# Optimization experiments

Measured on AMD Instinct MI355X. Metric: run time of the kernel, lower is better.

## Reference

```python
import jax, jax.numpy as jnp
import numpy as np

N_NODES = 100000
N_EDGES = 1600000
D = 128
BN_EPS = 1e-5

def setup_inputs() -> dict:
    key = jax.random.key(0)
    ks = jax.random.split(key, 6)
    h = jax.random.normal(ks[0], (N_NODES, D), dtype=jnp.float32)
    src = jax.random.randint(ks[1], (N_EDGES,), 0, N_NODES, dtype=jnp.int32)
    dst = jax.random.randint(ks[2], (N_EDGES,), 0, N_NODES, dtype=jnp.int32)
    eps = jnp.zeros((1,), dtype=jnp.float32)
    # 2-layer GIN apply_func MLP, scaled for stable activations
    W1 = jax.random.normal(ks[3], (D, D), dtype=jnp.float32) / np.sqrt(D)
    b1 = jnp.zeros((D,), dtype=jnp.float32)
    W2 = jax.random.normal(ks[4], (D, D), dtype=jnp.float32) / np.sqrt(D)
    b2 = jnp.zeros((D,), dtype=jnp.float32)
    gamma = jnp.ones((D,), dtype=jnp.float32)
    beta = jnp.zeros((D,), dtype=jnp.float32)
    return {"h": h, "src": src, "dst": dst, "eps": eps,
            "W1": W1, "b1": b1, "W2": W2, "b2": b2,
            "gamma": gamma, "beta": beta}

def reference(h, src, dst, eps, W1, b1, W2, b2, gamma, beta):
    # --- neighbor sum aggregation: update_all(copy_u('h'), fn.sum) ---
    msgs = h[src]                                   # [E, D] irregular gather
    neigh = jax.ops.segment_sum(msgs, dst, num_segments=N_NODES)  # [N, D]
    # --- eps-scaled self term ---
    x = (1.0 + eps[0]) * h + neigh                  # [N, D]
    # --- apply_func: 2-layer MLP ---
    x = jax.nn.relu(x @ W1 + b1)
    x = x @ W2 + b2
    # --- BatchNorm1d over node dim (training-mode batch stats) ---
    mean = jnp.mean(x, axis=0)
    var = jnp.mean(jnp.square(x - mean), axis=0)
    x = (x - mean) * jax.lax.rsqrt(var + BN_EPS) * gamma + beta
    # --- activation + residual ---
    x = jax.nn.relu(x)
    x = h + x  # residual (in_dim == out_dim)
    return x
```

## Files before the change

kernel.cpp:

```cpp
#include <hip/hip_runtime.h>

#define NN 100000
#define NE 1600000
#define DD 128
#define BN_EPS 1e-5f

#define NWIN 782
#define NWINP 1024
#define EPB 8192
#define NBLK ((NE + EPB - 1) / EPB)
#define CAP 3072
#define PREPBLKS 828
#define GRID_PS (NBLK + PREPBLKS)
#define BN_BLOCKS 1024

typedef __attribute__((ext_vector_type(8))) short short8;
typedef __attribute__((ext_vector_type(4))) float floatx4;

__device__ __forceinline__ unsigned short f2bf(float f) {
    union { float f; unsigned u; } v; v.f = f;
    return (unsigned short)((v.u + 0x7FFFu + ((v.u >> 16) & 1u)) >> 16);
}
__device__ __forceinline__ float bf2f(unsigned short u) {
    union { unsigned u; float f; } v; v.u = ((unsigned)u) << 16;
    return v.f;
}

__global__ __launch_bounds__(256) void prep_scatter_kernel(
    float* __restrict__ stats,
    const float* __restrict__ W1, const float* __restrict__ W2,
    unsigned short* __restrict__ W1t, unsigned short* __restrict__ W2t,
    const float* __restrict__ h, unsigned short* __restrict__ hb, int do_hb,
    const int* __restrict__ src, const int* __restrict__ dst,
    int* __restrict__ wcnt, int* __restrict__ estage)
{
    __shared__ int lofs[NWINP];
    __shared__ int lcur[NWINP];
    __shared__ int gbase[NWINP];
    __shared__ int sorted[EPB];
    __shared__ int stmp[256];
    int t = threadIdx.x;

    if (blockIdx.x < NBLK) {
        int blk = blockIdx.x;
        for (int w = t; w < NWINP; w += 256) lcur[w] = 0;
        __syncthreads();
        int base = blk * EPB;
        int cnt = min(EPB, NE - base);
        for (int i = t; i < cnt; i += 256)
            atomicAdd(&lcur[dst[base + i] >> 7], 1);
        __syncthreads();

        int w0 = t * 4;
        int c0 = lcur[w0], c1 = lcur[w0 + 1], c2 = lcur[w0 + 2], c3 = lcur[w0 + 3];
        int tsum = c0 + c1 + c2 + c3;
        stmp[t] = tsum;
        __syncthreads();
#pragma unroll
        for (int ofs = 1; ofs < 256; ofs <<= 1) {
            int u = (t >= ofs) ? stmp[t - ofs] : 0;
            __syncthreads();
            stmp[t] += u;
            __syncthreads();
        }
        int excl = stmp[t] - tsum;
        lofs[w0]     = excl;
        lofs[w0 + 1] = excl + c0;
        lofs[w0 + 2] = excl + c0 + c1;
        lofs[w0 + 3] = excl + c0 + c1 + c2;
        int gb0 = (w0     < NWIN && c0) ? atomicAdd(&wcnt[w0],     c0) : 0;
        int gb1 = (w0 + 1 < NWIN && c1) ? atomicAdd(&wcnt[w0 + 1], c1) : 0;
        int gb2 = (w0 + 2 < NWIN && c2) ? atomicAdd(&wcnt[w0 + 2], c2) : 0;
        int gb3 = (w0 + 3 < NWIN && c3) ? atomicAdd(&wcnt[w0 + 3], c3) : 0;
        gbase[w0]     = w0 * CAP + gb0;
        gbase[w0 + 1] = (w0 + 1) * CAP + gb1;
        gbase[w0 + 2] = (w0 + 2) * CAP + gb2;
        gbase[w0 + 3] = (w0 + 3) * CAP + gb3;
        lcur[w0] = lofs[w0]; lcur[w0 + 1] = lofs[w0 + 1];
        lcur[w0 + 2] = lofs[w0 + 2]; lcur[w0 + 3] = lofs[w0 + 3];
        __syncthreads();

        for (int i = t; i < cnt; i += 256) {
            int d = dst[base + i];
            int s = src[base + i];
            int p = atomicAdd(&lcur[d >> 7], 1);
            sorted[p] = (s << 7) | (d & 127);
        }
        __syncthreads();

        for (int w = t; w < NWIN; w += 256) {
            int lb = lofs[w], le = lcur[w];
            int g = gbase[w];
            for (int j = lb; j < le; ++j)
                estage[g + (j - lb)] = sorted[j];
        }
    } else {
        int tid0 = (blockIdx.x - NBLK) * 256 + t;
        int stride = PREPBLKS * 256;
        if (tid0 < 2 * DD) stats[tid0] = 0.0f;
        for (int i = tid0; i < DD * DD; i += stride) {
            int n = i >> 7, k = i & 127;
            W1t[i] = f2bf(W1[k * DD + n]);
            W2t[i] = f2bf(W2[k * DD + n]);
        }
        if (do_hb) {
            const float4* h4 = (const float4*)h;
            ushort4* hb4 = (ushort4*)hb;
            for (int i = tid0; i < NN * (DD / 4); i += stride) {
                float4 v = h4[i];
                ushort4 o;
                o.x = f2bf(v.x); o.y = f2bf(v.y); o.z = f2bf(v.z); o.w = f2bf(v.w);
                hb4[i] = o;
            }
        }
    }
}

template <bool HB>
__global__ __launch_bounds__(256) void permgather_kernel(
    const float* __restrict__ h, const unsigned short* __restrict__ hb,
    const float* __restrict__ eps, const int* __restrict__ wcnt,
    const int* __restrict__ estage, unsigned short* __restrict__ xb)
{
    __shared__ int es[CAP];
    __shared__ int cnt[128];
    __shared__ int beg[128];
    __shared__ int cur[128];
    __shared__ int dh[64];
    __shared__ int dcur[64];
    __shared__ unsigned char order[128];

    int b = blockIdx.x, t = threadIdx.x;
    if (t < 128) cnt[t] = 0;
    if (t < 64) dh[t] = 0;
    __syncthreads();

    int n = min(wcnt[b], CAP);
    int wbase = b * CAP;
    for (int i = t; i < n; i += 256)
        atomicAdd(&cnt[estage[wbase + i] & 127], 1);
    __syncthreads();

    if (t < 128) beg[t] = cnt[t];
    __syncthreads();
#pragma unroll
    for (int ofs = 1; ofs < 128; ofs <<= 1) {
        int u = (t < 128 && t >= ofs) ? beg[t - ofs] : 0;
        __syncthreads();
        if (t < 128) beg[t] += u;
        __syncthreads();
    }
    if (t < 128) {
        int ex = beg[t] - cnt[t];
        beg[t] = ex;
        cur[t] = ex;
        atomicAdd(&dh[min(cnt[t], 63)], 1);
    }
    __syncthreads();

    if (t < 64) dcur[t] = dh[t];
    __syncthreads();
#pragma unroll
    for (int ofs = 1; ofs < 64; ofs <<= 1) {
        int u = (t < 64 && t >= ofs) ? dcur[t - ofs] : 0;
        __syncthreads();
        if (t < 64) dcur[t] += u;
        __syncthreads();
    }
    if (t < 64) dcur[t] -= dh[t];
    __syncthreads();
    if (t < 128) {
        int p = atomicAdd(&dcur[min(cnt[t], 63)], 1);
        order[p] = (unsigned char)t;
    }
    __syncthreads();

    for (int i = t; i < n; i += 256) {
        int e = estage[wbase + i];
        int p = atomicAdd(&cur[e & 127], 1);
        es[p] = e >> 7;
    }
    __syncthreads();

    const float sE = 1.0f + eps[0];
    const float4* h4 = (const float4*)h;
    const short8* hb8 = (const short8*)hb;
    int c8 = t & 15;
#pragma unroll
    for (int pass = 0; pass < 8; ++pass) {
        int nl = order[pass * 16 + (t >> 4)];
        int node = (b << 7) + nl;
        if (node >= NN) continue;
        float4 a0 = h4[node * 32 + c8 * 2];
        float4 a1 = h4[node * 32 + c8 * 2 + 1];
        float acc[8] = {sE * a0.x, sE * a0.y, sE * a0.z, sE * a0.w,
                        sE * a1.x, sE * a1.y, sE * a1.z, sE * a1.w};
        int e = beg[nl], eend = beg[nl] + cnt[nl];
        if (HB) {
            for (; e + 3 < eend; e += 4) {
                int s0 = es[e], s1 = es[e + 1], s2 = es[e + 2], s3 = es[e + 3];
                short8 v0 = hb8[s0 * 16 + c8];
                short8 v1 = hb8[s1 * 16 + c8];
                short8 v2 = hb8[s2 * 16 + c8];
                short8 v3 = hb8[s3 * 16 + c8];
#pragma unroll
                for (int j = 0; j < 8; ++j) {
                    float t0 = bf2f((unsigned short)v0[j]) + bf2f((unsigned short)v1[j]);
                    float t1 = bf2f((unsigned short)v2[j]) + bf2f((unsigned short)v3[j]);
                    acc[j] += t0 + t1;
                }
            }
            for (; e < eend; ++e) {
                short8 v0 = hb8[es[e] * 16 + c8];
#pragma unroll
                for (int j = 0; j < 8; ++j) acc[j] += bf2f((unsigned short)v0[j]);
            }
        } else {
            for (; e + 1 < eend; e += 2) {
                int s0 = es[e], s1 = es[e + 1];
                float4 u0 = h4[s0 * 32 + c8 * 2], u1 = h4[s0 * 32 + c8 * 2 + 1];
                float4 w0 = h4[s1 * 32 + c8 * 2], w1 = h4[s1 * 32 + c8 * 2 + 1];
                acc[0] += u0.x + w0.x; acc[1] += u0.y + w0.y;
                acc[2] += u0.z + w0.z; acc[3] += u0.w + w0.w;
                acc[4] += u1.x + w1.x; acc[5] += u1.y + w1.y;
                acc[6] += u1.z + w1.z; acc[7] += u1.w + w1.w;
            }
            if (e < eend) {
                int s0 = es[e];
                float4 u0 = h4[s0 * 32 + c8 * 2], u1 = h4[s0 * 32 + c8 * 2 + 1];
                acc[0] += u0.x; acc[1] += u0.y; acc[2] += u0.z; acc[3] += u0.w;
                acc[4] += u1.x; acc[5] += u1.y; acc[6] += u1.z; acc[7] += u1.w;
            }
        }
        short8 o;
#pragma unroll
        for (int j = 0; j < 8; ++j) o[j] = (short)f2bf(acc[j]);
        ((short8*)xb)[node * 16 + c8] = o;
    }
}

__global__ __launch_bounds__(256) void mlp_fused_kernel(
    const unsigned short* __restrict__ X,
    const unsigned short* __restrict__ W1t, const unsigned short* __restrict__ W2t,
    const float* __restrict__ b1, const float* __restrict__ b2,
    unsigned short* __restrict__ Y, float* __restrict__ stats)
{
    extern __shared__ char smem[];
    unsigned short* wl = (unsigned short*)smem;
    unsigned short* xl = (unsigned short*)(smem + 34816);

    const int tid = threadIdx.x;
    const int r0 = blockIdx.x * 64;
    const int lane = tid & 63;
    const int wv = tid >> 6;
    const int m = lane & 15;
    const int hi = lane >> 4;

    const short8* W18 = (const short8*)W1t;
#pragma unroll
    for (int l = 0; l < 8; ++l) {
        int idx = tid + l * 256;
        int n = idx >> 4, c = idx & 15;
        *(short8*)&wl[n * 136 + c * 8] = W18[idx];
    }
    const short8* X8 = (const short8*)X;
#pragma unroll
    for (int l = 0; l < 4; ++l) {
        int idx = tid + l * 256;
        int row = idx >> 4, c = idx & 15;
        int g = r0 + row;
        short8 v = {0, 0, 0, 0, 0, 0, 0, 0};
        if (g < NN) v = X8[g * 16 + c];
        *(short8*)&xl[row * 136 + c * 8] = v;
    }
    __syncthreads();

    floatx4 acc[8];
#pragma unroll
    for (int i = 0; i < 8; ++i) acc[i] = (floatx4){0.f, 0.f, 0.f, 0.f};
#pragma unroll
    for (int kc = 0; kc < 4; ++kc) {
        short8 a = *(const short8*)&xl[(wv * 16 + m) * 136 + kc * 32 + hi * 8];
#pragma unroll
        for (int nt = 0; nt < 8; ++nt) {
            short8 b = *(const short8*)&wl[(nt * 16 + m) * 136 + kc * 32 + hi * 8];
            acc[nt] = __builtin_amdgcn_mfma_f32_16x16x32_bf16(a, b, acc[nt], 0, 0, 0);
        }
    }
    __syncthreads();

#pragma unroll
    for (int nt = 0; nt < 8; ++nt) {
        float bv = b1[nt * 16 + m];
#pragma unroll
        for (int r = 0; r < 4; ++r) {
            float v = fmaxf(acc[nt][r] + bv, 0.f);
            xl[(wv * 16 + hi * 4 + r) * 136 + nt * 16 + m] = f2bf(v);
        }
    }
    const short8* W28 = (const short8*)W2t;
#pragma unroll
    for (int l = 0; l < 8; ++l) {
        int idx = tid + l * 256;
        int n = idx >> 4, c = idx & 15;
        *(short8*)&wl[n * 136 + c * 8] = W28[idx];
    }
    __syncthreads();

#pragma unroll
    for (int i = 0; i < 8; ++i) acc[i] = (floatx4){0.f, 0.f, 0.f, 0.f};
#pragma unroll
    for (int kc = 0; kc < 4; ++kc) {
        short8 a = *(const short8*)&xl[(wv * 16 + m) * 136 + kc * 32 + hi * 8];
#pragma unroll
        for (int nt = 0; nt < 8; ++nt) {
            short8 b = *(const short8*)&wl[(nt * 16 + m) * 136 + kc * 32 + hi * 8];
            acc[nt] = __builtin_amdgcn_mfma_f32_16x16x32_bf16(a, b, acc[nt], 0, 0, 0);
        }
    }
    __syncthreads();

#pragma unroll
    for (int nt = 0; nt < 8; ++nt) {
        float bv = b2[nt * 16 + m];
#pragma unroll
        for (int r = 0; r < 4; ++r) {
            float v = acc[nt][r] + bv;
            xl[(wv * 16 + hi * 4 + r) * 136 + nt * 16 + m] = f2bf(v);
        }
    }
    __syncthreads();

#pragma unroll
    for (int l = 0; l < 4; ++l) {
        int idx = tid + l * 256;
        int row = idx >> 4, c = idx & 15;
        int g = r0 + row;
        if (g < NN)
            ((short8*)Y)[g * 16 + c] = *(const short8*)&xl[row * 136 + c * 8];
    }

    int col = tid & 127, half = tid >> 7;
    int rlim = min(64, NN - r0);
    int rbeg = half * 32, rend = min(rbeg + 32, rlim);
    float s = 0.f, q = 0.f;
    for (int r = rbeg; r < rend; ++r) {
        float v = bf2f(xl[r * 136 + col]);
        s += v; q += v * v;
    }
    float* red = (float*)wl;
    red[tid] = s;
    red[256 + tid] = q;
    __syncthreads();
    if (half == 0) {
        atomicAdd(&stats[col],      red[col] + red[128 + col]);
        atomicAdd(&stats[DD + col], red[256 + col] + red[256 + 128 + col]);
    }
}

__global__ __launch_bounds__(256) void bn_final_kernel(
    const unsigned short* __restrict__ Y, const float* __restrict__ h,
    const float* __restrict__ gamma, const float* __restrict__ beta,
    const float* __restrict__ stats, float* __restrict__ out)
{
    const float invN = 1.0f / (float)NN;
    int t0 = blockIdx.x * 256 + threadIdx.x;
    int c8 = t0 & 15;
    float sc[8], sh[8];
#pragma unroll
    for (int j = 0; j < 8; ++j) {
        int col = c8 * 8 + j;
        float mu = stats[col] * invN;
        float var = stats[DD + col] * invN - mu * mu;
        float s = rsqrtf(var + BN_EPS) * gamma[col];
        sc[j] = s;
        sh[j] = beta[col] - mu * s;
    }
    const short8* Y8 = (const short8*)Y;
    const float4* H4 = (const float4*)h;
    float4* O4 = (float4*)out;
    const int total = NN * 16;
    const int stride = BN_BLOCKS * 256;
    for (int i = t0; i < total; i += stride) {
        short8 u = Y8[i];
        float4 h0 = H4[2 * i], h1 = H4[2 * i + 1];
        float4 r0, r1;
        r0.x = h0.x + fmaxf(bf2f((unsigned short)u[0]) * sc[0] + sh[0], 0.f);
        r0.y = h0.y + fmaxf(bf2f((unsigned short)u[1]) * sc[1] + sh[1], 0.f);
        r0.z = h0.z + fmaxf(bf2f((unsigned short)u[2]) * sc[2] + sh[2], 0.f);
        r0.w = h0.w + fmaxf(bf2f((unsigned short)u[3]) * sc[3] + sh[3], 0.f);
        r1.x = h1.x + fmaxf(bf2f((unsigned short)u[4]) * sc[4] + sh[4], 0.f);
        r1.y = h1.y + fmaxf(bf2f((unsigned short)u[5]) * sc[5] + sh[5], 0.f);
        r1.z = h1.z + fmaxf(bf2f((unsigned short)u[6]) * sc[6] + sh[6], 0.f);
        r1.w = h1.w + fmaxf(bf2f((unsigned short)u[7]) * sc[7] + sh[7], 0.f);
        O4[2 * i] = r0;
        O4[2 * i + 1] = r1;
    }
}

extern "C" void kernel_launch(void* const* d_in, const int* in_sizes, int n_in,
                              void* d_out, int out_size, void* d_ws, size_t ws_size,
                              hipStream_t stream)
{
    const float* h     = (const float*)d_in[0];
    const int*   src   = (const int*)d_in[1];
    const int*   dst   = (const int*)d_in[2];
    const float* eps   = (const float*)d_in[3];
    const float* W1    = (const float*)d_in[4];
    const float* b1    = (const float*)d_in[5];
    const float* W2    = (const float*)d_in[6];
    const float* b2    = (const float*)d_in[7];
    const float* gamma = (const float*)d_in[8];
    const float* beta  = (const float*)d_in[9];
    float* out = (float*)d_out;

    char* w = (char*)d_ws;
    size_t o = 0;
    float* stats    = (float*)(w + o); o += 256 * 4;
    int* wcnt       = (int*)(w + o); o += 1024 * 4;
    unsigned short* W1t = (unsigned short*)(w + o); o += (size_t)DD * DD * 2;
    unsigned short* W2t = (unsigned short*)(w + o); o += (size_t)DD * DD * 2;
    int* estage     = (int*)(w + o); o += (size_t)NWIN * CAP * 4;
    unsigned short* xb  = (unsigned short*)(w + o); o += (size_t)NN * DD * 2;
    unsigned short* hb  = (unsigned short*)(w + o); o += (size_t)NN * DD * 2;
    const int use_hb = (ws_size >= o) ? 1 : 0;

    hipMemsetAsync(wcnt, 0, 1024 * sizeof(int), stream);

    prep_scatter_kernel<<<GRID_PS, 256, 0, stream>>>(
        stats, W1, W2, W1t, W2t, h, hb, use_hb, src, dst, wcnt, estage);

    if (use_hb)
        permgather_kernel<true><<<NWIN, 256, 0, stream>>>(h, hb, eps, wcnt, estage, xb);
    else
        permgather_kernel<false><<<NWIN, 256, 0, stream>>>(h, hb, eps, wcnt, estage, xb);

    int gemm_blocks = (NN + 63) / 64;
    size_t gemm_lds = 34816 + 17408;
    mlp_fused_kernel<<<gemm_blocks, 256, gemm_lds, stream>>>(xb, W1t, W2t, b1, b2, xb, stats);

    bn_final_kernel<<<BN_BLOCKS, 256, 0, stream>>>(xb, h, gamma, beta, stats, out);
}
```

Measured before the change: 296.6 us.

## Fuse neighbor gather with MLP GEMMs using 64-node windows

Destination windows shrink from 128 to 64 nodes so each gather block's output tile matches the MLP's 64-row tile. The gathered bf16 rows stay in LDS and feed both MFMA GEMMs directly, which removes the intermediate xb write/read round trip and one kernel launch. Weights are staged in two 64-row halves to fit LDS, and BN statistics are now accumulated from fp32 values instead of rounded bf16. The trade-off is twice as many scatter windows with a smaller per-window capacity (1536 edges), so an unusually dense window could overflow, and the gather and GEMM phases now share a single block's resources.

```diff
diff --git a/kernel.cpp b/kernel.cpp
--- a/kernel.cpp
+++ b/kernel.cpp
@@ -5,11 +5,13 @@
 #define DD 128
 #define BN_EPS 1e-5f
 
-#define NWIN 782
-#define NWINP 1024
+#define WSH 6
+#define WSZ 64
+#define NWIN ((NN + WSZ - 1) / WSZ)
+#define NWINP 2048
 #define EPB 8192
 #define NBLK ((NE + EPB - 1) / EPB)
-#define CAP 3072
+#define CAP 1536
 #define PREPBLKS 828
 #define GRID_PS (NBLK + PREPBLKS)
 #define BN_BLOCKS 1024
@@ -48,12 +50,14 @@
         int base = blk * EPB;
         int cnt = min(EPB, NE - base);
         for (int i = t; i < cnt; i += 256)
-            atomicAdd(&lcur[dst[base + i] >> 7], 1);
-        __syncthreads();
-
-        int w0 = t * 4;
-        int c0 = lcur[w0], c1 = lcur[w0 + 1], c2 = lcur[w0 + 2], c3 = lcur[w0 + 3];
-        int tsum = c0 + c1 + c2 + c3;
+            atomicAdd(&lcur[dst[base + i] >> WSH], 1);
+        __syncthreads();
+
+        int w0 = t * 8;
+        int c[8];
+        int tsum = 0;
+#pragma unroll
+        for (int j = 0; j < 8; ++j) { c[j] = lcur[w0 + j]; tsum += c[j]; }
         stmp[t] = tsum;
         __syncthreads();
 #pragma unroll
@@ -64,27 +68,22 @@
             __syncthreads();
         }
         int excl = stmp[t] - tsum;
-        lofs[w0]     = excl;
-        lofs[w0 + 1] = excl + c0;
-        lofs[w0 + 2] = excl + c0 + c1;
-        lofs[w0 + 3] = excl + c0 + c1 + c2;
-        int gb0 = (w0     < NWIN && c0) ? atomicAdd(&wcnt[w0],     c0) : 0;
-        int gb1 = (w0 + 1 < NWIN && c1) ? atomicAdd(&wcnt[w0 + 1], c1) : 0;
-        int gb2 = (w0 + 2 < NWIN && c2) ? atomicAdd(&wcnt[w0 + 2], c2) : 0;
-        int gb3 = (w0 + 3 < NWIN && c3) ? atomicAdd(&wcnt[w0 + 3], c3) : 0;
-        gbase[w0]     = w0 * CAP + gb0;
-        gbase[w0 + 1] = (w0 + 1) * CAP + gb1;
-        gbase[w0 + 2] = (w0 + 2) * CAP + gb2;
-        gbase[w0 + 3] = (w0 + 3) * CAP + gb3;
-        lcur[w0] = lofs[w0]; lcur[w0 + 1] = lofs[w0 + 1];
-        lcur[w0 + 2] = lofs[w0 + 2]; lcur[w0 + 3] = lofs[w0 + 3];
+#pragma unroll
+        for (int j = 0; j < 8; ++j) {
+            int w = w0 + j;
+            lofs[w] = excl;
+            lcur[w] = excl;
+            int gb = (w < NWIN && c[j]) ? atomicAdd(&wcnt[w], c[j]) : 0;
+            gbase[w] = w * CAP + gb;
+            excl += c[j];
+        }
         __syncthreads();
 
         for (int i = t; i < cnt; i += 256) {
             int d = dst[base + i];
             int s = src[base + i];
-            int p = atomicAdd(&lcur[d >> 7], 1);
-            sorted[p] = (s << 7) | (d & 127);
+            int p = atomicAdd(&lcur[d >> WSH], 1);
+            sorted[p] = (s << WSH) | (d & (WSZ - 1));
         }
         __syncthreads();
 
@@ -117,47 +116,58 @@
 }
 
 template <bool HB>
-__global__ __launch_bounds__(256) void permgather_kernel(
+__global__ __launch_bounds__(256) void permgather_mlp_kernel(
     const float* __restrict__ h, const unsigned short* __restrict__ hb,
     const float* __restrict__ eps, const int* __restrict__ wcnt,
-    const int* __restrict__ estage, unsigned short* __restrict__ xb)
+    const int* __restrict__ estage,
+    const unsigned short* __restrict__ W1t, const unsigned short* __restrict__ W2t,
+    const float* __restrict__ b1, const float* __restrict__ b2,
+    unsigned short* __restrict__ Y, float* __restrict__ stats)
 {
-    __shared__ int es[CAP];
-    __shared__ int cnt[128];
-    __shared__ int beg[128];
-    __shared__ int cur[128];
-    __shared__ int dh[64];
-    __shared__ int dcur[64];
-    __shared__ unsigned char order[128];
-
-    int b = blockIdx.x, t = threadIdx.x;
-    if (t < 128) cnt[t] = 0;
-    if (t < 64) dh[t] = 0;
-    __syncthreads();
-
+    __shared__ __align__(16) unsigned short xl[WSZ * 136];
+    __shared__ __align__(16) char un[17408];
+
+    int* es   = (int*)un;
+    int* cnt  = (int*)(un + 6144);
+    int* beg  = (int*)(un + 6144 + 256);
+    int* cur  = (int*)(un + 6144 + 512);
+    int* dh   = (int*)(un + 6144 + 768);
+    int* dcur = (int*)(un + 6144 + 1024);
+    unsigned char* order = (unsigned char*)(un + 6144 + 1280);
+    unsigned short* wl = (unsigned short*)un;
+    float* sred = (float*)un;
+    float* qred = sred + 2048;
+
+    const int b = blockIdx.x;
+    const int t = threadIdx.x;
+    const int lane = t & 63;
+    const int wv = t >> 6;
+    const int m = lane & 15;
+    const int hi = lane >> 4;
+
+    if (t < 64) { cnt[t] = 0; dh[t] = 0; }
+    __syncthreads();
     int n = min(wcnt[b], CAP);
     int wbase = b * CAP;
     for (int i = t; i < n; i += 256)
-        atomicAdd(&cnt[estage[wbase + i] & 127], 1);
-    __syncthreads();
-
-    if (t < 128) beg[t] = cnt[t];
-    __syncthreads();
-#pragma unroll
-    for (int ofs = 1; ofs < 128; ofs <<= 1) {
-        int u = (t < 128 && t >= ofs) ? beg[t - ofs] : 0;
-        __syncthreads();
-        if (t < 128) beg[t] += u;
-        __syncthreads();
-    }
-    if (t < 128) {
+        atomicAdd(&cnt[estage[wbase + i] & (WSZ - 1)], 1);
+    __syncthreads();
+    if (t < 64) beg[t] = cnt[t];
+    __syncthreads();
+#pragma unroll
+    for (int ofs = 1; ofs < 64; ofs <<= 1) {
+        int u = (t < 64 && t >= ofs) ? beg[t - ofs] : 0;
+        __syncthreads();
+        if (t < 64) beg[t] += u;
+        __syncthreads();
+    }
+    if (t < 64) {
         int ex = beg[t] - cnt[t];
         beg[t] = ex;
         cur[t] = ex;
         atomicAdd(&dh[min(cnt[t], 63)], 1);
     }
     __syncthreads();
-
     if (t < 64) dcur[t] = dh[t];
     __syncthreads();
 #pragma unroll
@@ -169,28 +179,31 @@
     }
     if (t < 64) dcur[t] -= dh[t];
     __syncthreads();
-    if (t < 128) {
+    if (t < 64) {
         int p = atomicAdd(&dcur[min(cnt[t], 63)], 1);
         order[p] = (unsigned char)t;
     }
     __syncthreads();
-
     for (int i = t; i < n; i += 256) {
         int e = estage[wbase + i];
-        int p = atomicAdd(&cur[e & 127], 1);
-        es[p] = e >> 7;
+        int p = atomicAdd(&cur[e & (WSZ - 1)], 1);
+        es[p] = e >> WSH;
     }
     __syncthreads();
 
     const float sE = 1.0f + eps[0];
     const float4* h4 = (const float4*)h;
     const short8* hb8 = (const short8*)hb;
-    int c8 = t & 15;
-#pragma unroll
-    for (int pass = 0; pass < 8; ++pass) {
+    const int c8 = t & 15;
+#pragma unroll
+    for (int pass = 0; pass < 4; ++pass) {
         int nl = order[pass * 16 + (t >> 4)];
-        int node = (b << 7) + nl;
-        if (node >= NN) continue;
+        int node = b * WSZ + nl;
+        if (node >= NN) {
+            short8 z = {0, 0, 0, 0, 0, 0, 0, 0};
+            *(short8*)&xl[nl * 136 + c8 * 8] = z;
+            continue;
+        }
         float4 a0 = h4[node * 32 + c8 * 2];
         float4 a1 = h4[node * 32 + c8 * 2 + 1];
         float acc[8] = {sE * a0.x, sE * a0.y, sE * a0.z, sE * a0.w,
@@ -235,60 +248,35 @@
         short8 o;
 #pragma unroll
         for (int j = 0; j < 8; ++j) o[j] = (short)f2bf(acc[j]);
-        ((short8*)xb)[node * 16 + c8] = o;
-    }
-}
-
-__global__ __launch_bounds__(256) void mlp_fused_kernel(
-    const unsigned short* __restrict__ X,
-    const unsigned short* __restrict__ W1t, const unsigned short* __restrict__ W2t,
-    const float* __restrict__ b1, const float* __restrict__ b2,
-    unsigned short* __restrict__ Y, float* __restrict__ stats)
-{
-    extern __shared__ char smem[];
-    unsigned short* wl = (unsigned short*)smem;
-    unsigned short* xl = (unsigned short*)(smem + 34816);
-
-    const int tid = threadIdx.x;
-    const int r0 = blockIdx.x * 64;
-    const int lane = tid & 63;
-    const int wv = tid >> 6;
-    const int m = lane & 15;
-    const int hi = lane >> 4;
-
-    const short8* W18 = (const short8*)W1t;
-#pragma unroll
-    for (int l = 0; l < 8; ++l) {
-        int idx = tid + l * 256;
-        int n = idx >> 4, c = idx & 15;
-        *(short8*)&wl[n * 136 + c * 8] = W18[idx];
-    }
-    const short8* X8 = (const short8*)X;
-#pragma unroll
-    for (int l = 0; l < 4; ++l) {
-        int idx = tid + l * 256;
-        int row = idx >> 4, c = idx & 15;
-        int g = r0 + row;
-        short8 v = {0, 0, 0, 0, 0, 0, 0, 0};
-        if (g < NN) v = X8[g * 16 + c];
-        *(short8*)&xl[row * 136 + c * 8] = v;
+        *(short8*)&xl[nl * 136 + c8 * 8] = o;
     }
     __syncthreads();
 
     floatx4 acc[8];
 #pragma unroll
     for (int i = 0; i < 8; ++i) acc[i] = (floatx4){0.f, 0.f, 0.f, 0.f};
-#pragma unroll
-    for (int kc = 0; kc < 4; ++kc) {
-        short8 a = *(const short8*)&xl[(wv * 16 + m) * 136 + kc * 32 + hi * 8];
-#pragma unroll
-        for (int nt = 0; nt < 8; ++nt) {
-            short8 b = *(const short8*)&wl[(nt * 16 + m) * 136 + kc * 32 + hi * 8];
-            acc[nt] = __builtin_amdgcn_mfma_f32_16x16x32_bf16(a, b, acc[nt], 0, 0, 0);
-        }
-    }
-    __syncthreads();
-
+    const short8* W1t8 = (const short8*)W1t;
+#pragma unroll
+    for (int hh = 0; hh < 2; ++hh) {
+#pragma unroll
+        for (int l = 0; l < 4; ++l) {
+            int idx = t + l * 256;
+            int nr = idx >> 4, c = idx & 15;
+            *(short8*)&wl[nr * 136 + c * 8] = W1t8[(hh * 64 + nr) * 16 + c];
+        }
+        __syncthreads();
+#pragma unroll
+        for (int kc = 0; kc < 4; ++kc) {
+            short8 a = *(const short8*)&xl[(wv * 16 + m) * 136 + kc * 32 + hi * 8];
+#pragma unroll
+            for (int ntl = 0; ntl < 4; ++ntl) {
+                short8 bb = *(const short8*)&wl[(ntl * 16 + m) * 136 + kc * 32 + hi * 8];
+                acc[hh * 4 + ntl] =
+                    __builtin_amdgcn_mfma_f32_16x16x32_bf16(a, bb, acc[hh * 4 + ntl], 0, 0, 0);
+            }
+        }
+        __syncthreads();
+    }
 #pragma unroll
     for (int nt = 0; nt < 8; ++nt) {
         float bv = b1[nt * 16 + m];
@@ -298,63 +286,63 @@
             xl[(wv * 16 + hi * 4 + r) * 136 + nt * 16 + m] = f2bf(v);
         }
     }
-    const short8* W28 = (const short8*)W2t;
-#pragma unroll
-    for (int l = 0; l < 8; ++l) {
-        int idx = tid + l * 256;
-        int n = idx >> 4, c = idx & 15;
-        *(short8*)&wl[n * 136 + c * 8] = W28[idx];
-    }
     __syncthreads();
 
 #pragma unroll
     for (int i = 0; i < 8; ++i) acc[i] = (floatx4){0.f, 0.f, 0.f, 0.f};
-#pragma unroll
-    for (int kc = 0; kc < 4; ++kc) {
-        short8 a = *(const short8*)&xl[(wv * 16 + m) * 136 + kc * 32 + hi * 8];
-#pragma unroll
-        for (int nt = 0; nt < 8; ++nt) {
-            short8 b = *(const short8*)&wl[(nt * 16 + m) * 136 + kc * 32 + hi * 8];
-            acc[nt] = __builtin_amdgcn_mfma_f32_16x16x32_bf16(a, b, acc[nt], 0, 0, 0);
-        }
-    }
-    __syncthreads();
+    const short8* W2t8 = (const short8*)W2t;
+#pragma unroll
+    for (int hh = 0; hh < 2; ++hh) {
+#pragma unroll
+        for (int l = 0; l < 4; ++l) {
+            int idx = t + l * 256;
+            int nr = idx >> 4, c = idx & 15;
+            *(short8*)&wl[nr * 136 + c * 8] = W2t8[(hh * 64 + nr) * 16 + c];
+        }
+        __syncthreads();
+#pragma unroll
+        for (int kc = 0; kc < 4; ++kc) {
+            short8 a = *(const short8*)&xl[(wv * 16 + m) * 136 + kc * 32 + hi * 8];
+#pragma unroll
+            for (int ntl = 0; ntl < 4; ++ntl) {
+                short8 bb = *(const short8*)&wl[(ntl * 16 + m) * 136 + kc * 32 + hi * 8];
+                acc[hh * 4 + ntl] =
+                    __builtin_amdgcn_mfma_f32_16x16x32_bf16(a, bb, acc[hh * 4 + ntl], 0, 0, 0);
+            }
+        }
+        __syncthreads();
+    }
 
 #pragma unroll
     for (int nt = 0; nt < 8; ++nt) {
         float bv = b2[nt * 16 + m];
+        float ss = 0.f, qq = 0.f;
 #pragma unroll
         for (int r = 0; r < 4; ++r) {
+            int row = wv * 16 + hi * 4 + r;
             float v = acc[nt][r] + bv;
-            xl[(wv * 16 + hi * 4 + r) * 136 + nt * 16 + m] = f2bf(v);
-        }
+            xl[row * 136 + nt * 16 + m] = f2bf(v);
+            if (b * WSZ + row < NN) { ss += v; qq += v * v; }
+        }
+        sred[(nt * 16 + m) * 16 + wv * 4 + hi] = ss;
+        qred[(nt * 16 + m) * 16 + wv * 4 + hi] = qq;
     }
     __syncthreads();
 
 #pragma unroll
     for (int l = 0; l < 4; ++l) {
-        int idx = tid + l * 256;
+        int idx = t + l * 256;
         int row = idx >> 4, c = idx & 15;
-        int g = r0 + row;
+        int g = b * WSZ + row;
         if (g < NN)
             ((short8*)Y)[g * 16 + c] = *(const short8*)&xl[row * 136 + c * 8];
     }
-
-    int col = tid & 127, half = tid >> 7;
-    int rlim = min(64, NN - r0);
-    int rbeg = half * 32, rend = min(rbeg + 32, rlim);
-    float s = 0.f, q = 0.f;
-    for (int r = rbeg; r < rend; ++r) {
-        float v = bf2f(xl[r * 136 + col]);
-        s += v; q += v * v;
-    }
-    float* red = (float*)wl;
-    red[tid] = s;
-    red[256 + tid] = q;
-    __syncthreads();
-    if (half == 0) {
-        atomicAdd(&stats[col],      red[col] + red[128 + col]);
-        atomicAdd(&stats[DD + col], red[256 + col] + red[256 + 128 + col]);
+    if (t < 128) {
+        float s = 0.f, q = 0.f;
+#pragma unroll
+        for (int j = 0; j < 16; ++j) { s += sred[t * 16 + j]; q += qred[t * 16 + j]; }
+        atomicAdd(&stats[t], s);
+        atomicAdd(&stats[DD + t], q);
     }
 }
 
@@ -417,7 +405,7 @@
     char* w = (char*)d_ws;
     size_t o = 0;
     float* stats    = (float*)(w + o); o += 256 * 4;
-    int* wcnt       = (int*)(w + o); o += 1024 * 4;
+    int* wcnt       = (int*)(w + o); o += NWINP * 4;
     unsigned short* W1t = (unsigned short*)(w + o); o += (size_t)DD * DD * 2;
     unsigned short* W2t = (unsigned short*)(w + o); o += (size_t)DD * DD * 2;
     int* estage     = (int*)(w + o); o += (size_t)NWIN * CAP * 4;
@@ -425,19 +413,17 @@
     unsigned short* hb  = (unsigned short*)(w + o); o += (size_t)NN * DD * 2;
     const int use_hb = (ws_size >= o) ? 1 : 0;
 
-    hipMemsetAsync(wcnt, 0, 1024 * sizeof(int), stream);
+    hipMemsetAsync(wcnt, 0, NWINP * sizeof(int), stream);
 
     prep_scatter_kernel<<<GRID_PS, 256, 0, stream>>>(
         stats, W1, W2, W1t, W2t, h, hb, use_hb, src, dst, wcnt, estage);
 
     if (use_hb)
-        permgather_kernel<true><<<NWIN, 256, 0, stream>>>(h, hb, eps, wcnt, estage, xb);
+        permgather_mlp_kernel<true><<<NWIN, 256, 0, stream>>>(
+            h, hb, eps, wcnt, estage, W1t, W2t, b1, b2, xb, stats);
     else
-        permgather_kernel<false><<<NWIN, 256, 0, stream>>>(h, hb, eps, wcnt, estage, xb);
-
-    int gemm_blocks = (NN + 63) / 64;
-    size_t gemm_lds = 34816 + 17408;
-    mlp_fused_kernel<<<gemm_blocks, 256, gemm_lds, stream>>>(xb, W1t, W2t, b1, b2, xb, stats);
+        permgather_mlp_kernel<false><<<NWIN, 256, 0, stream>>>(
+            h, hb, eps, wcnt, estage, W1t, W2t, b1, b2, xb, stats);
 
     bn_final_kernel<<<BN_BLOCKS, 256, 0, stream>>>(xb, h, gamma, beta, stats, out);
 }
```

After: 287.1 us. -3.2%, faster.
